# Performance work log

Hardware: AMD Instinct MI355X
Metric: run time of the kernel (lower is better)

Reference implementation:

```python
import jax, jax.numpy as jnp
import numpy as np

N_NODES = 100000
N_EDGES = 800000
F_IN = 128
HID = 128
HEADS = 4
HEAD_DIM = HID // HEADS
LAYERS = 3
N_CLASSES = 40
NEG_SLOPE = 0.2
BN_EPS = 1e-5


def setup_inputs() -> dict:
    key = jax.random.key(0)
    ks = jax.random.split(key, 10)
    feat = jax.random.normal(ks[0], (N_NODES, F_IN), dtype=jnp.float32)
    src = jax.random.randint(ks[1], (N_EDGES,), 0, N_NODES, dtype=jnp.int32)
    dst = jax.random.randint(ks[2], (N_EDGES,), 0, N_NODES, dtype=jnp.int32)
    W_enc = jax.random.normal(ks[3], (F_IN, HID), dtype=jnp.float32) / np.sqrt(F_IN)
    b_enc = jnp.zeros((HID,), dtype=jnp.float32)
    Ws = jax.random.normal(ks[4], (LAYERS, HID, HID), dtype=jnp.float32) / np.sqrt(HID)
    attn_ls = jax.random.normal(ks[5], (LAYERS, HEADS, HEAD_DIM), dtype=jnp.float32) / np.sqrt(HEAD_DIM)
    attn_rs = jax.random.normal(ks[6], (LAYERS, HEADS, HEAD_DIM), dtype=jnp.float32) / np.sqrt(HEAD_DIM)
    biases = jnp.zeros((LAYERS, HID), dtype=jnp.float32)
    gammas = jnp.ones((LAYERS, HID), dtype=jnp.float32)
    betas = jnp.zeros((LAYERS, HID), dtype=jnp.float32)
    W_pred = jax.random.normal(ks[7], (HID, N_CLASSES), dtype=jnp.float32) / np.sqrt(HID)
    b_pred = jnp.zeros((N_CLASSES,), dtype=jnp.float32)
    return {"feat": feat, "src": src, "dst": dst, "W_enc": W_enc, "b_enc": b_enc,
            "Ws": Ws, "attn_ls": attn_ls, "attn_rs": attn_rs, "biases": biases,
            "gammas": gammas, "betas": betas, "W_pred": W_pred, "b_pred": b_pred}


def _gat_layer(h, src, dst, W, a_l, a_r, bias, n_nodes):
    # h: [N, HID] -> projected per-head features [N, H, D]
    hf = (h @ W).reshape(n_nodes, HEADS, HEAD_DIM)
    el = jnp.sum(hf * a_l, axis=-1)  # [N, H]
    er = jnp.sum(hf * a_r, axis=-1)  # [N, H]
    e = jax.nn.leaky_relu(el[src] + er[dst], NEG_SLOPE)  # [E, H]
    # edge softmax over incoming edges of each destination node
    m = jax.ops.segment_max(e, dst, num_segments=n_nodes)  # [N, H]
    ex = jnp.exp(e - m[dst])
    s = jax.ops.segment_sum(ex, dst, num_segments=n_nodes)  # [N, H]
    alpha = ex / s[dst]  # [E, H]
    msg = hf[src] * alpha[:, :, None]  # [E, H, D]
    out = jax.ops.segment_sum(msg, dst, num_segments=n_nodes)  # [N, H, D]
    return out.reshape(n_nodes, HEADS * HEAD_DIM) + bias


def _batchnorm(x, gamma, beta):
    mean = jnp.mean(x, axis=0)
    var = jnp.var(x, axis=0)
    return gamma * (x - mean) * jax.lax.rsqrt(var + BN_EPS) + beta


def reference(feat, src, dst, W_enc, b_enc, Ws, attn_ls, attn_rs, biases, gammas, betas, W_pred, b_pred):
    n_nodes = feat.shape[0]
    h = jax.nn.relu(feat @ W_enc + b_enc)
    h_last = None
    for i in range(Ws.shape[0]):
        h = _gat_layer(h, src, dst, Ws[i], attn_ls[i], attn_rs[i], biases[i], n_nodes)
        if h_last is not None:
            h = h + h_last
        h_last = h
        h = _batchnorm(h, gammas[i], betas[i])
        h = jax.nn.relu(h)
    return h @ W_pred + b_pred
```

## Files before the change

### kernel.cpp

```cpp
#include <hip/hip_runtime.h>

typedef __attribute__((ext_vector_type(8))) short short8;
typedef __attribute__((ext_vector_type(4))) float f32x4;

#define N_NODES 100000
#define N_EDGES 800000
#define NEG 0.2f
#define BN_EPS 1e-5f
#define AGG_GRID 2048
#define MG_GRID 1024
#define MG_TILES 3125
#define SC_CHUNKS 256

__device__ __forceinline__ ushort bf16b(float f) {
  unsigned u = __float_as_uint(f);
  return (ushort)((u + 0x7FFFu + ((u >> 16) & 1u)) >> 16);
}
__device__ __forceinline__ float bflo(unsigned u) { return __uint_as_float(u << 16); }
__device__ __forceinline__ float bfhi(unsigned u) { return __uint_as_float(u & 0xFFFF0000u); }

__global__ void k_hist(const int* __restrict__ dst, int* __restrict__ cnt, int e) {
  int i = blockIdx.x * blockDim.x + threadIdx.x;
  if (i < e) atomicAdd(&cnt[dst[i]], 1);
}

__global__ void k_scan1(const int* __restrict__ cnt, int* __restrict__ rowptr,
                        int* __restrict__ bsums, int n) {
  __shared__ int sm[256];
  int i = blockIdx.x * 256 + threadIdx.x;
  int v = (i < n) ? cnt[i] : 0;
  sm[threadIdx.x] = v;
  __syncthreads();
  for (int off = 1; off < 256; off <<= 1) {
    int t = (threadIdx.x >= off) ? sm[threadIdx.x - off] : 0;
    __syncthreads();
    sm[threadIdx.x] += t;
    __syncthreads();
  }
  if (i < n) rowptr[i + 1] = sm[threadIdx.x];
  if (threadIdx.x == 255) bsums[blockIdx.x] = sm[255];
}

__global__ void k_scan2(int* __restrict__ bsums, int nb) {
  __shared__ int sm[512];
  int v = (threadIdx.x < nb) ? bsums[threadIdx.x] : 0;
  sm[threadIdx.x] = v;
  __syncthreads();
  for (int off = 1; off < 512; off <<= 1) {
    int t = (threadIdx.x >= off) ? sm[threadIdx.x - off] : 0;
    __syncthreads();
    sm[threadIdx.x] += t;
    __syncthreads();
  }
  if (threadIdx.x < nb) bsums[threadIdx.x] = sm[threadIdx.x] - v;
}

__global__ void k_scan3(int* __restrict__ rowptr, const int* __restrict__ bsums,
                        int* __restrict__ cursor, int n) {
  int i = blockIdx.x * 256 + threadIdx.x;
  if (i < n) {
    int val = rowptr[i + 1] + bsums[blockIdx.x];
    rowptr[i + 1] = val;
    if (i + 1 < n) cursor[i + 1] = val;
  }
  if (i == 0) { rowptr[0] = 0; cursor[0] = 0; }
}

__global__ __launch_bounds__(256) void k_scatter(
    const int* __restrict__ src, const int* __restrict__ dst,
    int* __restrict__ cursor, int2* __restrict__ esort, int e) {
  int xcd = blockIdx.x & 7;
  int chunk = blockIdx.x >> 3;
  int lo = xcd * (N_NODES / 8);
  int hi = lo + (N_NODES / 8);
  int per = (e + SC_CHUNKS - 1) / SC_CHUNKS;
  int beg = chunk * per;
  int end = min(e, beg + per);
  for (int i = beg + threadIdx.x; i < end; i += 256) {
    int d = dst[i];
    if (d >= lo && d < hi) {
      int pos = atomicAdd(&cursor[d], 1);
      esort[pos] = make_int2(src[i], d);
    }
  }
}

__global__ void k_packW(const float* __restrict__ W_enc, const float* __restrict__ Ws,
                        ushort* __restrict__ Wp) {
  int s = blockIdx.x * 256 + threadIdx.x;
  int wi = s >> 11, s2 = s & 2047;
  int kt = s2 >> 9, nb8 = (s2 >> 6) & 7, l = s2 & 63;
  const float* Wsrc = (wi == 0) ? W_enc : Ws + (size_t)(wi - 1) * 16384;
  int n = nb8 * 16 + (l & 15);
  int k0 = kt * 32 + (l >> 4) * 8;
  unsigned pk[4];
#pragma unroll
  for (int j = 0; j < 4; ++j) {
    ushort lo = bf16b(Wsrc[(size_t)(k0 + 2 * j) * 128 + n]);
    ushort hi = bf16b(Wsrc[(size_t)(k0 + 2 * j + 1) * 128 + n]);
    pk[j] = (unsigned)lo | ((unsigned)hi << 16);
  }
  *(uint4*)&Wp[(size_t)s * 8] = make_uint4(pk[0], pk[1], pk[2], pk[3]);
}

template <int MODE>
__global__ __launch_bounds__(256) void k_mgemm(
    const float* __restrict__ Af, const ushort* __restrict__ Ab,
    const ushort* __restrict__ Wp, const float* __restrict__ bias,
    const float* __restrict__ stats, const float* __restrict__ al,
    const float* __restrict__ ar, float* __restrict__ el, float* __restrict__ er,
    float4* __restrict__ blockmax, ushort* __restrict__ Cb) {
  __shared__ __align__(16) ushort Al[32 * 128];
  int tid = threadIdx.x;
  int lane = tid & 63, w = tid >> 6;
  int wr = w & 1, wc = w >> 1;
  int l15 = lane & 15, l4 = lane >> 4;

  const uint4* wp4 = (const uint4*)Wp;
  short8 bfr[4][4];
#pragma unroll
  for (int kt = 0; kt < 4; ++kt) {
#pragma unroll
    for (int nb = 0; nb < 4; ++nb) {
      uint4 t = wp4[(size_t)((kt * 8 + wc * 4 + nb) * 64 + lane)];
      bfr[kt][nb] = *(short8*)&t;
    }
  }

  float alv0 = 0, alv1 = 0, alv2 = 0, alv3 = 0;
  float arv0 = 0, arv1 = 0, arv2 = 0, arv3 = 0;
  float bv0 = 0, bv1 = 0, bv2 = 0, bv3 = 0;
  if (MODE != 0) {
    alv0 = al[64 * wc + l15];      arv0 = ar[64 * wc + l15];
    alv1 = al[64 * wc + 16 + l15]; arv1 = ar[64 * wc + 16 + l15];
    alv2 = al[64 * wc + 32 + l15]; arv2 = ar[64 * wc + 32 + l15];
    alv3 = al[64 * wc + 48 + l15]; arv3 = ar[64 * wc + 48 + l15];
  } else {
    bv0 = bias[64 * wc + l15];      bv1 = bias[64 * wc + 16 + l15];
    bv2 = bias[64 * wc + 32 + l15]; bv3 = bias[64 * wc + 48 + l15];
  }

  float gmx0 = -1e30f, gmx1 = -1e30f;

  int srow = tid >> 3;
  int c16 = (tid & 7) * 16;
  int kc0 = (tid & 7) * 2;
  int arow = 16 * wr + l15;
  const char* abase = (const char*)Al + arow * 256;
  int sw = arow & 7;

  for (int tile = blockIdx.x; tile < MG_TILES; tile += MG_GRID) {
    int rb = tile * 32;
    __syncthreads();
    {
      char* base = (char*)Al + srow * 256;
      if (MODE == 1) {
        const uint4* srcp = (const uint4*)(Ab + (size_t)(rb + srow) * 128 + c16);
        uint4 v0 = srcp[0], v1 = srcp[1];
        *(uint4*)(base + ((kc0 ^ (srow & 7)) << 4)) = v0;
        *(uint4*)(base + (((kc0 + 1) ^ (srow & 7)) << 4)) = v1;
      } else if (MODE == 2) {
        const uint4* srcp = (const uint4*)(Ab + (size_t)(rb + srow) * 128 + c16);
        uint4 v0 = srcp[0], v1 = srcp[1];
        unsigned pk[8];
#pragma unroll
        for (int j = 0; j < 4; ++j) {
          unsigned wv = ((const unsigned*)&v0)[j];
          float2 sc = *(const float2*)&stats[c16 + 2 * j];
          float2 sh = *(const float2*)&stats[128 + c16 + 2 * j];
          float x0 = fmaxf(bflo(wv) * sc.x + sh.x, 0.f);
          float x1 = fmaxf(bfhi(wv) * sc.y + sh.y, 0.f);
          pk[j] = (unsigned)bf16b(x0) | ((unsigned)bf16b(x1) << 16);
        }
#pragma unroll
        for (int j = 0; j < 4; ++j) {
          unsigned wv = ((const unsigned*)&v1)[j];
          float2 sc = *(const float2*)&stats[c16 + 8 + 2 * j];
          float2 sh = *(const float2*)&stats[128 + c16 + 8 + 2 * j];
          float x0 = fmaxf(bflo(wv) * sc.x + sh.x, 0.f);
          float x1 = fmaxf(bfhi(wv) * sc.y + sh.y, 0.f);
          pk[4 + j] = (unsigned)bf16b(x0) | ((unsigned)bf16b(x1) << 16);
        }
        *(uint4*)(base + ((kc0 ^ (srow & 7)) << 4)) = make_uint4(pk[0], pk[1], pk[2], pk[3]);
        *(uint4*)(base + (((kc0 + 1) ^ (srow & 7)) << 4)) = make_uint4(pk[4], pk[5], pk[6], pk[7]);
      } else {
        const float4* srcp = (const float4*)(Af + (size_t)(rb + srow) * 128 + c16);
        float4 f[4];
#pragma unroll
        for (int j = 0; j < 4; ++j) f[j] = srcp[j];
        unsigned pk[8];
#pragma unroll
        for (int j = 0; j < 4; ++j) {
          pk[2 * j] = (unsigned)bf16b(f[j].x) | ((unsigned)bf16b(f[j].y) << 16);
          pk[2 * j + 1] = (unsigned)bf16b(f[j].z) | ((unsigned)bf16b(f[j].w) << 16);
        }
        *(uint4*)(base + ((kc0 ^ (srow & 7)) << 4)) = make_uint4(pk[0], pk[1], pk[2], pk[3]);
        *(uint4*)(base + (((kc0 + 1) ^ (srow & 7)) << 4)) = make_uint4(pk[4], pk[5], pk[6], pk[7]);
      }
    }
    __syncthreads();

    f32x4 acc[4];
#pragma unroll
    for (int nb = 0; nb < 4; ++nb) acc[nb] = (f32x4){0.f, 0.f, 0.f, 0.f};
#pragma unroll
    for (int kt = 0; kt < 4; ++kt) {
      short8 af = *(const short8*)(abase + (((kt * 4 + l4) ^ sw) << 4));
      acc[0] = __builtin_amdgcn_mfma_f32_16x16x32_bf16(af, bfr[kt][0], acc[0], 0, 0, 0);
      acc[1] = __builtin_amdgcn_mfma_f32_16x16x32_bf16(af, bfr[kt][1], acc[1], 0, 0, 0);
      acc[2] = __builtin_amdgcn_mfma_f32_16x16x32_bf16(af, bfr[kt][2], acc[2], 0, 0, 0);
      acc[3] = __builtin_amdgcn_mfma_f32_16x16x32_bf16(af, bfr[kt][3], acc[3], 0, 0, 0);
    }

    int row0 = rb + 16 * wr + 4 * l4;
#pragma unroll
    for (int i = 0; i < 4; ++i) {
      int row = row0 + i;
      if (MODE != 0) {
        float pl0 = acc[0][i] * alv0 + acc[1][i] * alv1;
        float pr0 = acc[0][i] * arv0 + acc[1][i] * arv1;
        float pl1 = acc[2][i] * alv2 + acc[3][i] * alv3;
        float pr1 = acc[2][i] * arv2 + acc[3][i] * arv3;
#pragma unroll
        for (int o = 1; o < 16; o <<= 1) {
          pl0 += __shfl_xor(pl0, o); pr0 += __shfl_xor(pr0, o);
          pl1 += __shfl_xor(pl1, o); pr1 += __shfl_xor(pr1, o);
        }
        gmx0 = fmaxf(gmx0, pl0); gmx1 = fmaxf(gmx1, pl1);
        if (l15 == 0) {
          el[(size_t)row * 4 + 2 * wc] = pl0;     er[(size_t)row * 4 + 2 * wc] = pr0;
          el[(size_t)row * 4 + 2 * wc + 1] = pl1; er[(size_t)row * 4 + 2 * wc + 1] = pr1;
        }
      }
      float v0 = acc[0][i], v1 = acc[1][i], v2 = acc[2][i], v3 = acc[3][i];
      if (MODE == 0) {
        v0 = fmaxf(v0 + bv0, 0.f); v1 = fmaxf(v1 + bv1, 0.f);
        v2 = fmaxf(v2 + bv2, 0.f); v3 = fmaxf(v3 + bv3, 0.f);
      }
      size_t rbase = (size_t)row * 128 + 64 * wc + l15;
      Cb[rbase] = bf16b(v0);
      Cb[rbase + 16] = bf16b(v1);
      Cb[rbase + 32] = bf16b(v2);
      Cb[rbase + 48] = bf16b(v3);
    }
  }

  if (MODE != 0) {
    gmx0 = fmaxf(gmx0, __shfl_xor(gmx0, 16)); gmx0 = fmaxf(gmx0, __shfl_xor(gmx0, 32));
    gmx1 = fmaxf(gmx1, __shfl_xor(gmx1, 16)); gmx1 = fmaxf(gmx1, __shfl_xor(gmx1, 32));
    __shared__ float lm[4][2];
    if (lane == 0) { lm[w][0] = gmx0; lm[w][1] = gmx1; }
    __syncthreads();
    if (tid == 0) {
      float4 bm;
      bm.x = fmaxf(lm[0][0], lm[1][0]);
      bm.y = fmaxf(lm[0][1], lm[1][1]);
      bm.z = fmaxf(lm[2][0], lm[3][0]);
      bm.w = fmaxf(lm[2][1], lm[3][1]);
      blockmax[blockIdx.x] = bm;
    }
  }
}

__global__ __launch_bounds__(256) void k_elmax2(const float4* __restrict__ bm,
                                                float* __restrict__ elmax, int g) {
  float4 m = make_float4(-1e30f, -1e30f, -1e30f, -1e30f);
  for (int i = threadIdx.x; i < g; i += 256) {
    float4 v = bm[i];
    m.x = fmaxf(m.x, v.x); m.y = fmaxf(m.y, v.y);
    m.z = fmaxf(m.z, v.z); m.w = fmaxf(m.w, v.w);
  }
  __shared__ float4 sm[256];
  sm[threadIdx.x] = m;
  __syncthreads();
  for (int off = 128; off; off >>= 1) {
    if (threadIdx.x < off) {
      float4 o = sm[threadIdx.x + off];
      sm[threadIdx.x].x = fmaxf(sm[threadIdx.x].x, o.x);
      sm[threadIdx.x].y = fmaxf(sm[threadIdx.x].y, o.y);
      sm[threadIdx.x].z = fmaxf(sm[threadIdx.x].z, o.z);
      sm[threadIdx.x].w = fmaxf(sm[threadIdx.x].w, o.w);
    }
    __syncthreads();
  }
  if (threadIdx.x == 0) {
    elmax[0] = sm[0].x; elmax[1] = sm[0].y;
    elmax[2] = sm[0].z; elmax[3] = sm[0].w;
  }
}

__global__ __launch_bounds__(256) void k_edgew(
    const int2* __restrict__ esort, const float* __restrict__ el,
    const float* __restrict__ er, const float* __restrict__ elmax,
    float4* __restrict__ wgt, int e) {
  int j = blockIdx.x * 256 + threadIdx.x;
  if (j >= e) return;
  int2 sd = esort[j];
  float4 elv = *(const float4*)&el[(size_t)4 * sd.x];
  float4 erv = *(const float4*)&er[(size_t)4 * sd.y];
  float m0 = elmax[0] + erv.x;
  float m1 = elmax[1] + erv.y;
  float m2 = elmax[2] + erv.z;
  float m3 = elmax[3] + erv.w;
  m0 = fmaxf(m0, NEG * m0); m1 = fmaxf(m1, NEG * m1);
  m2 = fmaxf(m2, NEG * m2); m3 = fmaxf(m3, NEG * m3);
  float e0 = elv.x + erv.x; e0 = fmaxf(e0, NEG * e0);
  float e1 = elv.y + erv.y; e1 = fmaxf(e1, NEG * e1);
  float e2 = elv.z + erv.z; e2 = fmaxf(e2, NEG * e2);
  float e3 = elv.w + erv.w; e3 = fmaxf(e3, NEG * e3);
  float4 wv;
  wv.x = __expf(e0 - m0); wv.y = __expf(e1 - m1);
  wv.z = __expf(e2 - m2); wv.w = __expf(e3 - m3);
  wgt[j] = wv;
}

__global__ __launch_bounds__(256, 8) void k_aggregate(
    const ushort* __restrict__ hf, const float4* __restrict__ wgt,
    const int* __restrict__ rowptr, const int2* __restrict__ esort,
    const float* __restrict__ bias, ushort* __restrict__ hpre,
    float* __restrict__ part, int n, int addres) {
  int tid = threadIdx.x;
  int w = tid >> 6, lane = tid & 63;
  int h = lane >> 4;
  int c0 = 2 * lane;
  float2 bb = *(const float2*)&bias[c0];
  float sbn0 = 0.f, sbn1 = 0.f, qbn0 = 0.f, qbn1 = 0.f;
  for (int wid = blockIdx.x * 4 + w; wid < n; wid += AGG_GRID * 4) {
    int beg = rowptr[wid], end = rowptr[wid + 1];
    float s0 = 0.f, a00 = 0.f, a10 = 0.f;
    float s1 = 0.f, a01 = 0.f, a11 = 0.f;
    float s2 = 0.f, a02 = 0.f, a12 = 0.f;
    float s3 = 0.f, a03 = 0.f, a13 = 0.f;
    int j = beg;
    for (; j + 4 <= end; j += 4) {
      int sA = esort[j].x, sB = esort[j + 1].x, sC = esort[j + 2].x, sD = esort[j + 3].x;
      float wA = ((const float*)(wgt + j))[h];
      float wB = ((const float*)(wgt + j + 1))[h];
      float wC = ((const float*)(wgt + j + 2))[h];
      float wD = ((const float*)(wgt + j + 3))[h];
      unsigned hA = *(const unsigned*)(hf + (size_t)sA * 128 + c0);
      unsigned hB = *(const unsigned*)(hf + (size_t)sB * 128 + c0);
      unsigned hC = *(const unsigned*)(hf + (size_t)sC * 128 + c0);
      unsigned hD = *(const unsigned*)(hf + (size_t)sD * 128 + c0);
      s0 += wA; a00 += wA * bflo(hA); a10 += wA * bfhi(hA);
      s1 += wB; a01 += wB * bflo(hB); a11 += wB * bfhi(hB);
      s2 += wC; a02 += wC * bflo(hC); a12 += wC * bfhi(hC);
      s3 += wD; a03 += wD * bflo(hD); a13 += wD * bfhi(hD);
    }
    if (j < end) {
      int jB = (j + 1 < end) ? j + 1 : j;
      int jC = (j + 2 < end) ? j + 2 : j;
      int jD = (j + 3 < end) ? j + 3 : j;
      int sA = esort[j].x, sB = esort[jB].x, sC = esort[jC].x, sD = esort[jD].x;
      float wA = ((const float*)(wgt + j))[h];
      float wB = (j + 1 < end) ? ((const float*)(wgt + jB))[h] : 0.f;
      float wC = (j + 2 < end) ? ((const float*)(wgt + jC))[h] : 0.f;
      float wD = (j + 3 < end) ? ((const float*)(wgt + jD))[h] : 0.f;
      unsigned hA = *(const unsigned*)(hf + (size_t)sA * 128 + c0);
      unsigned hB = *(const unsigned*)(hf + (size_t)sB * 128 + c0);
      unsigned hC = *(const unsigned*)(hf + (size_t)sC * 128 + c0);
      unsigned hD = *(const unsigned*)(hf + (size_t)sD * 128 + c0);
      s0 += wA; a00 += wA * bflo(hA); a10 += wA * bfhi(hA);
      s1 += wB; a01 += wB * bflo(hB); a11 += wB * bfhi(hB);
      s2 += wC; a02 += wC * bflo(hC); a12 += wC * bfhi(hC);
      s3 += wD; a03 += wD * bflo(hD); a13 += wD * bfhi(hD);
    }
    float s = (s0 + s1) + (s2 + s3);
    float inv = (end > beg) ? 1.f / s : 0.f;
    float a0 = ((a00 + a01) + (a02 + a03)) * inv;
    float a1 = ((a10 + a11) + (a12 + a13)) * inv;
    float r0 = 0.f, r1 = 0.f;
    if (addres) {
      unsigned rr = *(const unsigned*)(hpre + (size_t)wid * 128 + c0);
      r0 = bflo(rr); r1 = bfhi(rr);
    }
    float o0 = a0 + bb.x + r0, o1 = a1 + bb.y + r1;
    *(unsigned*)(hpre + (size_t)wid * 128 + c0) =
        (unsigned)bf16b(o0) | ((unsigned)bf16b(o1) << 16);
    sbn0 += o0; qbn0 += o0 * o0;
    sbn1 += o1; qbn1 += o1 * o1;
  }
  __shared__ float red_s[4][128];
  __shared__ float red_q[4][128];
  red_s[w][c0] = sbn0; red_s[w][c0 + 1] = sbn1;
  red_q[w][c0] = qbn0; red_q[w][c0 + 1] = qbn1;
  __syncthreads();
  if (tid < 128)
    part[(size_t)blockIdx.x * 256 + tid] =
        (red_s[0][tid] + red_s[1][tid]) + (red_s[2][tid] + red_s[3][tid]);
  else if (tid < 256) {
    int c = tid - 128;
    part[(size_t)blockIdx.x * 256 + tid] =
        (red_q[0][c] + red_q[1][c]) + (red_q[2][c] + red_q[3][c]);
  }
}

__global__ __launch_bounds__(320) void k_pred(
    const ushort* __restrict__ A, const float* __restrict__ stats,
    const float* __restrict__ W, const float* __restrict__ bias,
    float* __restrict__ out, int n) {
  __shared__ float Wl[128 * 40];
  __shared__ float Xl[32 * 132];
  for (int i = threadIdx.x; i < 128 * 40; i += 320) Wl[i] = W[i];
  int cg = threadIdx.x % 10;
  int rg = threadIdx.x / 10;
  float4 bv = *(const float4*)&bias[4 * cg];
  for (int rb = blockIdx.x * 32; rb < n; rb += gridDim.x * 32) {
    __syncthreads();
    for (int idx = threadIdx.x; idx < 1024; idx += 320) {
      int r = idx >> 5, c = (idx & 31) * 4;
      uint2 v = *(const uint2*)(A + (size_t)(rb + r) * 128 + c);
      float4 sc = *(const float4*)&stats[c];
      float4 sh = *(const float4*)&stats[128 + c];
      float x0 = fmaxf(bflo(v.x) * sc.x + sh.x, 0.f);
      float x1 = fmaxf(bfhi(v.x) * sc.y + sh.y, 0.f);
      float x2 = fmaxf(bflo(v.y) * sc.z + sh.z, 0.f);
      float x3 = fmaxf(bfhi(v.y) * sc.w + sh.w, 0.f);
      *(float4*)&Xl[r * 132 + c] = make_float4(x0, x1, x2, x3);
    }
    __syncthreads();
    float a0 = 0.f, a1 = 0.f, a2 = 0.f, a3 = 0.f;
#pragma unroll 4
    for (int k = 0; k < 128; ++k) {
      float x = Xl[rg * 132 + k];
      float4 w = *(float4*)&Wl[k * 40 + 4 * cg];
      a0 += x * w.x; a1 += x * w.y; a2 += x * w.z; a3 += x * w.w;
    }
    float4 o = make_float4(a0 + bv.x, a1 + bv.y, a2 + bv.z, a3 + bv.w);
    *(float4*)&out[(size_t)(rb + rg) * 40 + 4 * cg] = o;
  }
}

__global__ __launch_bounds__(256) void k_bnred(
    const float* __restrict__ part, float* __restrict__ colsum,
    const float* __restrict__ gamma, const float* __restrict__ beta,
    float* __restrict__ stats, unsigned* __restrict__ ctr, int g, int n) {
  int v = blockIdx.x;
  float acc = 0.f;
  for (int b = threadIdx.x; b < g; b += 256) acc += part[(size_t)b * 256 + v];
  __shared__ float sm[256];
  sm[threadIdx.x] = acc;
  __syncthreads();
  for (int off = 128; off; off >>= 1) {
    if (threadIdx.x < off) sm[threadIdx.x] += sm[threadIdx.x + off];
    __syncthreads();
  }
  __shared__ int last;
  if (threadIdx.x == 0) {
    colsum[v] = sm[0];
    __threadfence();
    last = (atomicAdd(ctr, 1u) == (unsigned)(gridDim.x - 1));
  }
  __syncthreads();
  if (last) {
    __threadfence();
    if (threadIdx.x == 0) *ctr = 0;
    if (threadIdx.x < 128) {
      int c = threadIdx.x;
      float mean = colsum[c] / n;
      float var = colsum[128 + c] / n - mean * mean;
      float rstd = rsqrtf(var + BN_EPS);
      float scale = gamma[c] * rstd;
      stats[c] = scale;
      stats[128 + c] = beta[c] - mean * scale;
    }
  }
}

extern "C" void kernel_launch(void* const* d_in, const int* in_sizes, int n_in,
                              void* d_out, int out_size, void* d_ws, size_t ws_size,
                              hipStream_t stream) {
  const float* feat   = (const float*)d_in[0];
  const int*   src    = (const int*)d_in[1];
  const int*   dst    = (const int*)d_in[2];
  const float* W_enc  = (const float*)d_in[3];
  const float* b_enc  = (const float*)d_in[4];
  const float* Ws     = (const float*)d_in[5];
  const float* a_ls   = (const float*)d_in[6];
  const float* a_rs   = (const float*)d_in[7];
  const float* biases = (const float*)d_in[8];
  const float* gammas = (const float*)d_in[9];
  const float* betas  = (const float*)d_in[10];
  const float* W_pred = (const float*)d_in[11];
  const float* b_pred = (const float*)d_in[12];
  float* out = (float*)d_out;

  char* p = (char*)d_ws;
  auto alloc = [&](size_t bytes) {
    char* q = p;
    p += (bytes + 255) & ~(size_t)255;
    return q;
  };
  ushort* h_bf  = (ushort*)alloc((size_t)N_NODES * 128 * 2);
  ushort* hf_bf = (ushort*)alloc((size_t)N_NODES * 128 * 2);
  ushort* hpre  = (ushort*)alloc((size_t)N_NODES * 128 * 2);
  float* el     = (float*)alloc((size_t)N_NODES * 4 * 4);
  float* er     = (float*)alloc((size_t)N_NODES * 4 * 4);
  float* part   = (float*)alloc((size_t)AGG_GRID * 256 * 4);
  float* colsum = (float*)alloc(256 * 4);
  float* stats  = (float*)alloc(256 * 4);
  ushort* Wpack = (ushort*)alloc((size_t)4 * 2048 * 16);
  float4* bmax  = (float4*)alloc((size_t)MG_GRID * 16);
  float* elmax  = (float*)alloc(4 * 4);
  unsigned* ctr = (unsigned*)alloc(256);
  int* rowptr   = (int*)alloc((size_t)(N_NODES + 1) * 4);
  int* cursor   = (int*)alloc((size_t)N_NODES * 4);
  int* bsums    = (int*)alloc(512 * 4);
  int2* esort   = (int2*)alloc((size_t)N_EDGES * 8);
  float4* wgt   = (float4*)alloc((size_t)N_EDGES * 16);

  hipMemsetAsync(cursor, 0, (size_t)N_NODES * 4, stream);
  hipMemsetAsync(ctr, 0, 8, stream);
  k_hist<<<(N_EDGES + 255) / 256, 256, 0, stream>>>(dst, cursor, N_EDGES);
  int nb = (N_NODES + 255) / 256;
  k_scan1<<<nb, 256, 0, stream>>>(cursor, rowptr, bsums, N_NODES);
  k_scan2<<<1, 512, 0, stream>>>(bsums, nb);
  k_scan3<<<nb, 256, 0, stream>>>(rowptr, bsums, cursor, N_NODES);
  k_scatter<<<SC_CHUNKS * 8, 256, 0, stream>>>(src, dst, cursor, esort, N_EDGES);

  k_packW<<<32, 256, 0, stream>>>(W_enc, Ws, Wpack);

  k_mgemm<0><<<MG_GRID, 256, 0, stream>>>(feat, nullptr, Wpack, b_enc, nullptr, nullptr,
                                          nullptr, nullptr, nullptr, nullptr, h_bf);

  for (int L = 0; L < 3; ++L) {
    const float* al = a_ls + L * 128;
    const float* ar = a_rs + L * 128;
    const ushort* wp = Wpack + (size_t)(1 + L) * 16384;
    if (L == 0)
      k_mgemm<1><<<MG_GRID, 256, 0, stream>>>(nullptr, h_bf, wp, nullptr, nullptr, al,
                                              ar, el, er, bmax, hf_bf);
    else
      k_mgemm<2><<<MG_GRID, 256, 0, stream>>>(nullptr, hpre, wp, nullptr, stats, al,
                                              ar, el, er, bmax, hf_bf);
    k_elmax2<<<1, 256, 0, stream>>>(bmax, elmax, MG_GRID);
    k_edgew<<<(N_EDGES + 255) / 256, 256, 0, stream>>>(esort, el, er, elmax, wgt,
                                                       N_EDGES);
    k_aggregate<<<AGG_GRID, 256, 0, stream>>>(hf_bf, wgt, rowptr, esort,
                                              biases + L * 128, hpre, part, N_NODES,
                                              L > 0 ? 1 : 0);
    k_bnred<<<256, 256, 0, stream>>>(part, colsum, gammas + L * 128, betas + L * 128,
                                     stats, ctr, AGG_GRID, N_NODES);
  }
  k_pred<<<1563, 320, 0, stream>>>(hpre, stats, W_pred, b_pred, out, N_NODES);
}
```

Baseline: 407.6 us.

## Fuse encoder GEMM into first GAT projection and use MFMA for predictor

The encoder matmul and the layer-0 projection now run in one kernel. The ReLU'd encoder output stays in shared memory as bf16 instead of making a round trip through a global h buffer. The final predictor is rewritten as a bf16 MFMA GEMM with a packed, zero-padded W_pred, replacing the scalar FP32 LDS loop. The cost is more registers in the fused kernel, which holds two weight fragment sets, and bf16 rounding in the predictor.

```diff
diff --git a/kernel.cpp b/kernel.cpp
--- a/kernel.cpp
+++ b/kernel.cpp
@@ -103,6 +103,168 @@
   *(uint4*)&Wp[(size_t)s * 8] = make_uint4(pk[0], pk[1], pk[2], pk[3]);
 }
 
+__global__ void k_packP(const float* __restrict__ Wpred, ushort* __restrict__ Wp) {
+  int s = blockIdx.x * 256 + threadIdx.x;
+  if (s >= 1024) return;
+  int kt = s >> 8, nb = (s >> 6) & 3, l = s & 63;
+  int n = nb * 16 + (l & 15);
+  int k0 = kt * 32 + (l >> 4) * 8;
+  unsigned pk[4];
+#pragma unroll
+  for (int j = 0; j < 4; ++j) {
+    float lo = (n < 40) ? Wpred[(size_t)(k0 + 2 * j) * 40 + n] : 0.f;
+    float hi = (n < 40) ? Wpred[(size_t)(k0 + 2 * j + 1) * 40 + n] : 0.f;
+    pk[j] = (unsigned)bf16b(lo) | ((unsigned)bf16b(hi) << 16);
+  }
+  *(uint4*)&Wp[(size_t)s * 8] = make_uint4(pk[0], pk[1], pk[2], pk[3]);
+}
+
+__global__ __launch_bounds__(256) void k_fused(
+    const float* __restrict__ feat, const ushort* __restrict__ WpE,
+    const ushort* __restrict__ Wp0, const float* __restrict__ b_enc,
+    const float* __restrict__ al, const float* __restrict__ ar,
+    float* __restrict__ el, float* __restrict__ er,
+    float4* __restrict__ blockmax, ushort* __restrict__ Cb) {
+  __shared__ __align__(16) ushort Al[32 * 128];
+  __shared__ __align__(16) ushort A2[32 * 128];
+  int tid = threadIdx.x;
+  int lane = tid & 63, w = tid >> 6;
+  int wr = w & 1, wc = w >> 1;
+  int l15 = lane & 15, l4 = lane >> 4;
+
+  const uint4* wpE4 = (const uint4*)WpE;
+  const uint4* wp04 = (const uint4*)Wp0;
+  short8 bfrE[4][4], bfr0[4][4];
+#pragma unroll
+  for (int kt = 0; kt < 4; ++kt) {
+#pragma unroll
+    for (int nb = 0; nb < 4; ++nb) {
+      uint4 tE = wpE4[(size_t)((kt * 8 + wc * 4 + nb) * 64 + lane)];
+      bfrE[kt][nb] = *(short8*)&tE;
+      uint4 t0 = wp04[(size_t)((kt * 8 + wc * 4 + nb) * 64 + lane)];
+      bfr0[kt][nb] = *(short8*)&t0;
+    }
+  }
+
+  float bv0 = b_enc[64 * wc + l15],      bv1 = b_enc[64 * wc + 16 + l15];
+  float bv2 = b_enc[64 * wc + 32 + l15], bv3 = b_enc[64 * wc + 48 + l15];
+  float alv0 = al[64 * wc + l15],      arv0 = ar[64 * wc + l15];
+  float alv1 = al[64 * wc + 16 + l15], arv1 = ar[64 * wc + 16 + l15];
+  float alv2 = al[64 * wc + 32 + l15], arv2 = ar[64 * wc + 32 + l15];
+  float alv3 = al[64 * wc + 48 + l15], arv3 = ar[64 * wc + 48 + l15];
+
+  float gmx0 = -1e30f, gmx1 = -1e30f;
+  int srow = tid >> 3;
+  int c16 = (tid & 7) * 16;
+  int kc0 = (tid & 7) * 2;
+  int arow = 16 * wr + l15;
+  const char* abase = (const char*)Al + arow * 256;
+  const char* abase2 = (const char*)A2 + arow * 256;
+  int sw = arow & 7;
+
+  for (int tile = blockIdx.x; tile < MG_TILES; tile += MG_GRID) {
+    int rb = tile * 32;
+    __syncthreads();
+    {
+      char* base = (char*)Al + srow * 256;
+      const float4* srcp = (const float4*)(feat + (size_t)(rb + srow) * 128 + c16);
+      float4 f[4];
+#pragma unroll
+      for (int j = 0; j < 4; ++j) f[j] = srcp[j];
+      unsigned pk[8];
+#pragma unroll
+      for (int j = 0; j < 4; ++j) {
+        pk[2 * j] = (unsigned)bf16b(f[j].x) | ((unsigned)bf16b(f[j].y) << 16);
+        pk[2 * j + 1] = (unsigned)bf16b(f[j].z) | ((unsigned)bf16b(f[j].w) << 16);
+      }
+      *(uint4*)(base + ((kc0 ^ (srow & 7)) << 4)) = make_uint4(pk[0], pk[1], pk[2], pk[3]);
+      *(uint4*)(base + (((kc0 + 1) ^ (srow & 7)) << 4)) = make_uint4(pk[4], pk[5], pk[6], pk[7]);
+    }
+    __syncthreads();
+
+    f32x4 acc[4];
+#pragma unroll
+    for (int nb = 0; nb < 4; ++nb) acc[nb] = (f32x4){0.f, 0.f, 0.f, 0.f};
+#pragma unroll
+    for (int kt = 0; kt < 4; ++kt) {
+      short8 af = *(const short8*)(abase + (((kt * 4 + l4) ^ sw) << 4));
+      acc[0] = __builtin_amdgcn_mfma_f32_16x16x32_bf16(af, bfrE[kt][0], acc[0], 0, 0, 0);
+      acc[1] = __builtin_amdgcn_mfma_f32_16x16x32_bf16(af, bfrE[kt][1], acc[1], 0, 0, 0);
+      acc[2] = __builtin_amdgcn_mfma_f32_16x16x32_bf16(af, bfrE[kt][2], acc[2], 0, 0, 0);
+      acc[3] = __builtin_amdgcn_mfma_f32_16x16x32_bf16(af, bfrE[kt][3], acc[3], 0, 0, 0);
+    }
+    {
+      int rl0 = 16 * wr + 4 * l4;
+#pragma unroll
+      for (int i = 0; i < 4; ++i) {
+        int rl = rl0 + i;
+        int sw2 = rl & 7;
+        char* b2 = (char*)A2 + rl * 256;
+#pragma unroll
+        for (int nb = 0; nb < 4; ++nb) {
+          int col = 64 * wc + 16 * nb + l15;
+          float bv = (nb == 0) ? bv0 : (nb == 1) ? bv1 : (nb == 2) ? bv2 : bv3;
+          float v = fmaxf(acc[nb][i] + bv, 0.f);
+          int chunk = col >> 3;
+          *(ushort*)(b2 + (((chunk ^ sw2) << 4) | ((col & 7) * 2))) = bf16b(v);
+        }
+      }
+    }
+    __syncthreads();
+
+    f32x4 acc2[4];
+#pragma unroll
+    for (int nb = 0; nb < 4; ++nb) acc2[nb] = (f32x4){0.f, 0.f, 0.f, 0.f};
+#pragma unroll
+    for (int kt = 0; kt < 4; ++kt) {
+      short8 af = *(const short8*)(abase2 + (((kt * 4 + l4) ^ sw) << 4));
+      acc2[0] = __builtin_amdgcn_mfma_f32_16x16x32_bf16(af, bfr0[kt][0], acc2[0], 0, 0, 0);
+      acc2[1] = __builtin_amdgcn_mfma_f32_16x16x32_bf16(af, bfr0[kt][1], acc2[1], 0, 0, 0);
+      acc2[2] = __builtin_amdgcn_mfma_f32_16x16x32_bf16(af, bfr0[kt][2], acc2[2], 0, 0, 0);
+      acc2[3] = __builtin_amdgcn_mfma_f32_16x16x32_bf16(af, bfr0[kt][3], acc2[3], 0, 0, 0);
+    }
+
+    int row0 = rb + 16 * wr + 4 * l4;
+#pragma unroll
+    for (int i = 0; i < 4; ++i) {
+      int row = row0 + i;
+      float pl0 = acc2[0][i] * alv0 + acc2[1][i] * alv1;
+      float pr0 = acc2[0][i] * arv0 + acc2[1][i] * arv1;
+      float pl1 = acc2[2][i] * alv2 + acc2[3][i] * alv3;
+      float pr1 = acc2[2][i] * arv2 + acc2[3][i] * arv3;
+#pragma unroll
+      for (int o = 1; o < 16; o <<= 1) {
+        pl0 += __shfl_xor(pl0, o); pr0 += __shfl_xor(pr0, o);
+        pl1 += __shfl_xor(pl1, o); pr1 += __shfl_xor(pr1, o);
+      }
+      gmx0 = fmaxf(gmx0, pl0); gmx1 = fmaxf(gmx1, pl1);
+      if (l15 == 0) {
+        el[(size_t)row * 4 + 2 * wc] = pl0;     er[(size_t)row * 4 + 2 * wc] = pr0;
+        el[(size_t)row * 4 + 2 * wc + 1] = pl1; er[(size_t)row * 4 + 2 * wc + 1] = pr1;
+      }
+      size_t rbase = (size_t)row * 128 + 64 * wc + l15;
+      Cb[rbase] = bf16b(acc2[0][i]);
+      Cb[rbase + 16] = bf16b(acc2[1][i]);
+      Cb[rbase + 32] = bf16b(acc2[2][i]);
+      Cb[rbase + 48] = bf16b(acc2[3][i]);
+    }
+  }
+
+  gmx0 = fmaxf(gmx0, __shfl_xor(gmx0, 16)); gmx0 = fmaxf(gmx0, __shfl_xor(gmx0, 32));
+  gmx1 = fmaxf(gmx1, __shfl_xor(gmx1, 16)); gmx1 = fmaxf(gmx1, __shfl_xor(gmx1, 32));
+  __shared__ float lm[4][2];
+  if (lane == 0) { lm[w][0] = gmx0; lm[w][1] = gmx1; }
+  __syncthreads();
+  if (tid == 0) {
+    float4 bm;
+    bm.x = fmaxf(lm[0][0], lm[1][0]);
+    bm.y = fmaxf(lm[0][1], lm[1][1]);
+    bm.z = fmaxf(lm[2][0], lm[3][0]);
+    bm.w = fmaxf(lm[2][1], lm[3][1]);
+    blockmax[blockIdx.x] = bm;
+  }
+}
+
 template <int MODE>
 __global__ __launch_bounds__(256) void k_mgemm(
     const float* __restrict__ Af, const ushort* __restrict__ Ab,
@@ -127,21 +289,12 @@
     }
   }
 
-  float alv0 = 0, alv1 = 0, alv2 = 0, alv3 = 0;
-  float arv0 = 0, arv1 = 0, arv2 = 0, arv3 = 0;
-  float bv0 = 0, bv1 = 0, bv2 = 0, bv3 = 0;
-  if (MODE != 0) {
-    alv0 = al[64 * wc + l15];      arv0 = ar[64 * wc + l15];
-    alv1 = al[64 * wc + 16 + l15]; arv1 = ar[64 * wc + 16 + l15];
-    alv2 = al[64 * wc + 32 + l15]; arv2 = ar[64 * wc + 32 + l15];
-    alv3 = al[64 * wc + 48 + l15]; arv3 = ar[64 * wc + 48 + l15];
-  } else {
-    bv0 = bias[64 * wc + l15];      bv1 = bias[64 * wc + 16 + l15];
-    bv2 = bias[64 * wc + 32 + l15]; bv3 = bias[64 * wc + 48 + l15];
-  }
+  float alv0 = al[64 * wc + l15],      arv0 = ar[64 * wc + l15];
+  float alv1 = al[64 * wc + 16 + l15], arv1 = ar[64 * wc + 16 + l15];
+  float alv2 = al[64 * wc + 32 + l15], arv2 = ar[64 * wc + 32 + l15];
+  float alv3 = al[64 * wc + 48 + l15], arv3 = ar[64 * wc + 48 + l15];
 
   float gmx0 = -1e30f, gmx1 = -1e30f;
-
   int srow = tid >> 3;
   int c16 = (tid & 7) * 16;
   int kc0 = (tid & 7) * 2;
@@ -154,49 +307,29 @@
     __syncthreads();
     {
       char* base = (char*)Al + srow * 256;
-      if (MODE == 1) {
-        const uint4* srcp = (const uint4*)(Ab + (size_t)(rb + srow) * 128 + c16);
-        uint4 v0 = srcp[0], v1 = srcp[1];
-        *(uint4*)(base + ((kc0 ^ (srow & 7)) << 4)) = v0;
-        *(uint4*)(base + (((kc0 + 1) ^ (srow & 7)) << 4)) = v1;
-      } else if (MODE == 2) {
-        const uint4* srcp = (const uint4*)(Ab + (size_t)(rb + srow) * 128 + c16);
-        uint4 v0 = srcp[0], v1 = srcp[1];
-        unsigned pk[8];
-#pragma unroll
-        for (int j = 0; j < 4; ++j) {
-          unsigned wv = ((const unsigned*)&v0)[j];
-          float2 sc = *(const float2*)&stats[c16 + 2 * j];
-          float2 sh = *(const float2*)&stats[128 + c16 + 2 * j];
-          float x0 = fmaxf(bflo(wv) * sc.x + sh.x, 0.f);
-          float x1 = fmaxf(bfhi(wv) * sc.y + sh.y, 0.f);
-          pk[j] = (unsigned)bf16b(x0) | ((unsigned)bf16b(x1) << 16);
-        }
-#pragma unroll
-        for (int j = 0; j < 4; ++j) {
-          unsigned wv = ((const unsigned*)&v1)[j];
-          float2 sc = *(const float2*)&stats[c16 + 8 + 2 * j];
-          float2 sh = *(const float2*)&stats[128 + c16 + 8 + 2 * j];
-          float x0 = fmaxf(bflo(wv) * sc.x + sh.x, 0.f);
-          float x1 = fmaxf(bfhi(wv) * sc.y + sh.y, 0.f);
-          pk[4 + j] = (unsigned)bf16b(x0) | ((unsigned)bf16b(x1) << 16);
-        }
-        *(uint4*)(base + ((kc0 ^ (srow & 7)) << 4)) = make_uint4(pk[0], pk[1], pk[2], pk[3]);
-        *(uint4*)(base + (((kc0 + 1) ^ (srow & 7)) << 4)) = make_uint4(pk[4], pk[5], pk[6], pk[7]);
-      } else {
-        const float4* srcp = (const float4*)(Af + (size_t)(rb + srow) * 128 + c16);
-        float4 f[4];
-#pragma unroll
-        for (int j = 0; j < 4; ++j) f[j] = srcp[j];
-        unsigned pk[8];
-#pragma unroll
-        for (int j = 0; j < 4; ++j) {
-          pk[2 * j] = (unsigned)bf16b(f[j].x) | ((unsigned)bf16b(f[j].y) << 16);
-          pk[2 * j + 1] = (unsigned)bf16b(f[j].z) | ((unsigned)bf16b(f[j].w) << 16);
-        }
-        *(uint4*)(base + ((kc0 ^ (srow & 7)) << 4)) = make_uint4(pk[0], pk[1], pk[2], pk[3]);
-        *(uint4*)(base + (((kc0 + 1) ^ (srow & 7)) << 4)) = make_uint4(pk[4], pk[5], pk[6], pk[7]);
-      }
+      const uint4* srcp = (const uint4*)(Ab + (size_t)(rb + srow) * 128 + c16);
+      uint4 v0 = srcp[0], v1 = srcp[1];
+      unsigned pk[8];
+#pragma unroll
+      for (int j = 0; j < 4; ++j) {
+        unsigned wv = ((const unsigned*)&v0)[j];
+        float2 sc = *(const float2*)&stats[c16 + 2 * j];
+        float2 sh = *(const float2*)&stats[128 + c16 + 2 * j];
+        float x0 = fmaxf(bflo(wv) * sc.x + sh.x, 0.f);
+        float x1 = fmaxf(bfhi(wv) * sc.y + sh.y, 0.f);
+        pk[j] = (unsigned)bf16b(x0) | ((unsigned)bf16b(x1) << 16);
+      }
+#pragma unroll
+      for (int j = 0; j < 4; ++j) {
+        unsigned wv = ((const unsigned*)&v1)[j];
+        float2 sc = *(const float2*)&stats[c16 + 8 + 2 * j];
+        float2 sh = *(const float2*)&stats[128 + c16 + 8 + 2 * j];
+        float x0 = fmaxf(bflo(wv) * sc.x + sh.x, 0.f);
+        float x1 = fmaxf(bfhi(wv) * sc.y + sh.y, 0.f);
+        pk[4 + j] = (unsigned)bf16b(x0) | ((unsigned)bf16b(x1) << 16);
+      }
+      *(uint4*)(base + ((kc0 ^ (srow & 7)) << 4)) = make_uint4(pk[0], pk[1], pk[2], pk[3]);
+      *(uint4*)(base + (((kc0 + 1) ^ (srow & 7)) << 4)) = make_uint4(pk[4], pk[5], pk[6], pk[7]);
     }
     __syncthreads();
 
@@ -216,49 +349,40 @@
 #pragma unroll
     for (int i = 0; i < 4; ++i) {
       int row = row0 + i;
-      if (MODE != 0) {
-        float pl0 = acc[0][i] * alv0 + acc[1][i] * alv1;
-        float pr0 = acc[0][i] * arv0 + acc[1][i] * arv1;
-        float pl1 = acc[2][i] * alv2 + acc[3][i] * alv3;
-        float pr1 = acc[2][i] * arv2 + acc[3][i] * arv3;
-#pragma unroll
-        for (int o = 1; o < 16; o <<= 1) {
-          pl0 += __shfl_xor(pl0, o); pr0 += __shfl_xor(pr0, o);
-          pl1 += __shfl_xor(pl1, o); pr1 += __shfl_xor(pr1, o);
-        }
-        gmx0 = fmaxf(gmx0, pl0); gmx1 = fmaxf(gmx1, pl1);
-        if (l15 == 0) {
-          el[(size_t)row * 4 + 2 * wc] = pl0;     er[(size_t)row * 4 + 2 * wc] = pr0;
-          el[(size_t)row * 4 + 2 * wc + 1] = pl1; er[(size_t)row * 4 + 2 * wc + 1] = pr1;
-        }
-      }
-      float v0 = acc[0][i], v1 = acc[1][i], v2 = acc[2][i], v3 = acc[3][i];
-      if (MODE == 0) {
-        v0 = fmaxf(v0 + bv0, 0.f); v1 = fmaxf(v1 + bv1, 0.f);
-        v2 = fmaxf(v2 + bv2, 0.f); v3 = fmaxf(v3 + bv3, 0.f);
+      float pl0 = acc[0][i] * alv0 + acc[1][i] * alv1;
+      float pr0 = acc[0][i] * arv0 + acc[1][i] * arv1;
+      float pl1 = acc[2][i] * alv2 + acc[3][i] * alv3;
+      float pr1 = acc[2][i] * arv2 + acc[3][i] * arv3;
+#pragma unroll
+      for (int o = 1; o < 16; o <<= 1) {
+        pl0 += __shfl_xor(pl0, o); pr0 += __shfl_xor(pr0, o);
+        pl1 += __shfl_xor(pl1, o); pr1 += __shfl_xor(pr1, o);
+      }
+      gmx0 = fmaxf(gmx0, pl0); gmx1 = fmaxf(gmx1, pl1);
+      if (l15 == 0) {
+        el[(size_t)row * 4 + 2 * wc] = pl0;     er[(size_t)row * 4 + 2 * wc] = pr0;
+        el[(size_t)row * 4 + 2 * wc + 1] = pl1; er[(size_t)row * 4 + 2 * wc + 1] = pr1;
       }
       size_t rbase = (size_t)row * 128 + 64 * wc + l15;
-      Cb[rbase] = bf16b(v0);
-      Cb[rbase + 16] = bf16b(v1);
-      Cb[rbase + 32] = bf16b(v2);
-      Cb[rbase + 48] = bf16b(v3);
-    }
-  }
-
-  if (MODE != 0) {
-    gmx0 = fmaxf(gmx0, __shfl_xor(gmx0, 16)); gmx0 = fmaxf(gmx0, __shfl_xor(gmx0, 32));
-    gmx1 = fmaxf(gmx1, __shfl_xor(gmx1, 16)); gmx1 = fmaxf(gmx1, __shfl_xor(gmx1, 32));
-    __shared__ float lm[4][2];
-    if (lane == 0) { lm[w][0] = gmx0; lm[w][1] = gmx1; }
-    __syncthreads();
-    if (tid == 0) {
-      float4 bm;
-      bm.x = fmaxf(lm[0][0], lm[1][0]);
-      bm.y = fmaxf(lm[0][1], lm[1][1]);
-      bm.z = fmaxf(lm[2][0], lm[3][0]);
-      bm.w = fmaxf(lm[2][1], lm[3][1]);
-      blockmax[blockIdx.x] = bm;
-    }
+      Cb[rbase] = bf16b(acc[0][i]);
+      Cb[rbase + 16] = bf16b(acc[1][i]);
+      Cb[rbase + 32] = bf16b(acc[2][i]);
+      Cb[rbase + 48] = bf16b(acc[3][i]);
+    }
+  }
+
+  gmx0 = fmaxf(gmx0, __shfl_xor(gmx0, 16)); gmx0 = fmaxf(gmx0, __shfl_xor(gmx0, 32));
+  gmx1 = fmaxf(gmx1, __shfl_xor(gmx1, 16)); gmx1 = fmaxf(gmx1, __shfl_xor(gmx1, 32));
+  __shared__ float lm[4][2];
+  if (lane == 0) { lm[w][0] = gmx0; lm[w][1] = gmx1; }
+  __syncthreads();
+  if (tid == 0) {
+    float4 bm;
+    bm.x = fmaxf(lm[0][0], lm[1][0]);
+    bm.y = fmaxf(lm[0][1], lm[1][1]);
+    bm.z = fmaxf(lm[2][0], lm[3][0]);
+    bm.w = fmaxf(lm[2][1], lm[3][1]);
+    blockmax[blockIdx.x] = bm;
   }
 }
 
@@ -395,39 +519,84 @@
   }
 }
 
-__global__ __launch_bounds__(320) void k_pred(
+__global__ __launch_bounds__(256) void k_predm(
     const ushort* __restrict__ A, const float* __restrict__ stats,
-    const float* __restrict__ W, const float* __restrict__ bias,
-    float* __restrict__ out, int n) {
-  __shared__ float Wl[128 * 40];
-  __shared__ float Xl[32 * 132];
-  for (int i = threadIdx.x; i < 128 * 40; i += 320) Wl[i] = W[i];
-  int cg = threadIdx.x % 10;
-  int rg = threadIdx.x / 10;
-  float4 bv = *(const float4*)&bias[4 * cg];
-  for (int rb = blockIdx.x * 32; rb < n; rb += gridDim.x * 32) {
-    __syncthreads();
-    for (int idx = threadIdx.x; idx < 1024; idx += 320) {
-      int r = idx >> 5, c = (idx & 31) * 4;
-      uint2 v = *(const uint2*)(A + (size_t)(rb + r) * 128 + c);
-      float4 sc = *(const float4*)&stats[c];
-      float4 sh = *(const float4*)&stats[128 + c];
-      float x0 = fmaxf(bflo(v.x) * sc.x + sh.x, 0.f);
-      float x1 = fmaxf(bfhi(v.x) * sc.y + sh.y, 0.f);
-      float x2 = fmaxf(bflo(v.y) * sc.z + sh.z, 0.f);
-      float x3 = fmaxf(bfhi(v.y) * sc.w + sh.w, 0.f);
-      *(float4*)&Xl[r * 132 + c] = make_float4(x0, x1, x2, x3);
-    }
-    __syncthreads();
-    float a0 = 0.f, a1 = 0.f, a2 = 0.f, a3 = 0.f;
-#pragma unroll 4
-    for (int k = 0; k < 128; ++k) {
-      float x = Xl[rg * 132 + k];
-      float4 w = *(float4*)&Wl[k * 40 + 4 * cg];
-      a0 += x * w.x; a1 += x * w.y; a2 += x * w.z; a3 += x * w.w;
-    }
-    float4 o = make_float4(a0 + bv.x, a1 + bv.y, a2 + bv.z, a3 + bv.w);
-    *(float4*)&out[(size_t)(rb + rg) * 40 + 4 * cg] = o;
+    const ushort* __restrict__ Wp, const float* __restrict__ bias,
+    float* __restrict__ out) {
+  __shared__ __align__(16) ushort Al[32 * 128];
+  int tid = threadIdx.x;
+  int lane = tid & 63, w = tid >> 6;
+  int wr = w & 1, wc = w >> 1;
+  int l15 = lane & 15, l4 = lane >> 4;
+
+  const uint4* wp4 = (const uint4*)Wp;
+  short8 bfrP[4][2];
+#pragma unroll
+  for (int kt = 0; kt < 4; ++kt) {
+#pragma unroll
+    for (int n = 0; n < 2; ++n) {
+      uint4 t = wp4[(size_t)((kt * 4 + wc * 2 + n) * 64 + lane)];
+      bfrP[kt][n] = *(short8*)&t;
+    }
+  }
+  int col0 = 32 * wc + l15, col1 = 32 * wc + 16 + l15;
+  float bp0 = (col0 < 40) ? bias[col0] : 0.f;
+  float bp1 = (col1 < 40) ? bias[col1] : 0.f;
+
+  int srow = tid >> 3;
+  int c16 = (tid & 7) * 16;
+  int kc0 = (tid & 7) * 2;
+  int arow = 16 * wr + l15;
+  const char* abase = (const char*)Al + arow * 256;
+  int sw = arow & 7;
+
+  for (int tile = blockIdx.x; tile < MG_TILES; tile += MG_GRID) {
+    int rb = tile * 32;
+    __syncthreads();
+    {
+      char* base = (char*)Al + srow * 256;
+      const uint4* srcp = (const uint4*)(A + (size_t)(rb + srow) * 128 + c16);
+      uint4 v0 = srcp[0], v1 = srcp[1];
+      unsigned pk[8];
+#pragma unroll
+      for (int j = 0; j < 4; ++j) {
+        unsigned wv = ((const unsigned*)&v0)[j];
+        float2 sc = *(const float2*)&stats[c16 + 2 * j];
+        float2 sh = *(const float2*)&stats[128 + c16 + 2 * j];
+        float x0 = fmaxf(bflo(wv) * sc.x + sh.x, 0.f);
+        float x1 = fmaxf(bfhi(wv) * sc.y + sh.y, 0.f);
+        pk[j] = (unsigned)bf16b(x0) | ((unsigned)bf16b(x1) << 16);
+      }
+#pragma unroll
+      for (int j = 0; j < 4; ++j) {
+        unsigned wv = ((const unsigned*)&v1)[j];
+        float2 sc = *(const float2*)&stats[c16 + 8 + 2 * j];
+        float2 sh = *(const float2*)&stats[128 + c16 + 8 + 2 * j];
+        float x0 = fmaxf(bflo(wv) * sc.x + sh.x, 0.f);
+        float x1 = fmaxf(bfhi(wv) * sc.y + sh.y, 0.f);
+        pk[4 + j] = (unsigned)bf16b(x0) | ((unsigned)bf16b(x1) << 16);
+      }
+      *(uint4*)(base + ((kc0 ^ (srow & 7)) << 4)) = make_uint4(pk[0], pk[1], pk[2], pk[3]);
+      *(uint4*)(base + (((kc0 + 1) ^ (srow & 7)) << 4)) = make_uint4(pk[4], pk[5], pk[6], pk[7]);
+    }
+    __syncthreads();
+
+    f32x4 acc0 = (f32x4){0.f, 0.f, 0.f, 0.f};
+    f32x4 acc1 = (f32x4){0.f, 0.f, 0.f, 0.f};
+#pragma unroll
+    for (int kt = 0; kt < 4; ++kt) {
+      short8 af = *(const short8*)(abase + (((kt * 4 + l4) ^ sw) << 4));
+      acc0 = __builtin_amdgcn_mfma_f32_16x16x32_bf16(af, bfrP[kt][0], acc0, 0, 0, 0);
+      acc1 = __builtin_amdgcn_mfma_f32_16x16x32_bf16(af, bfrP[kt][1], acc1, 0, 0, 0);
+    }
+
+    int row0 = rb + 16 * wr + 4 * l4;
+#pragma unroll
+    for (int i = 0; i < 4; ++i) {
+      int row = row0 + i;
+      if (col0 < 40) out[(size_t)row * 40 + col0] = acc0[i] + bp0;
+      if (col1 < 40) out[(size_t)row * 40 + col1] = acc1[i] + bp1;
+    }
   }
 }
 
@@ -491,7 +660,6 @@
     p += (bytes + 255) & ~(size_t)255;
     return q;
   };
-  ushort* h_bf  = (ushort*)alloc((size_t)N_NODES * 128 * 2);
   ushort* hf_bf = (ushort*)alloc((size_t)N_NODES * 128 * 2);
   ushort* hpre  = (ushort*)alloc((size_t)N_NODES * 128 * 2);
   float* el     = (float*)alloc((size_t)N_NODES * 4 * 4);
@@ -500,6 +668,7 @@
   float* colsum = (float*)alloc(256 * 4);
   float* stats  = (float*)alloc(256 * 4);
   ushort* Wpack = (ushort*)alloc((size_t)4 * 2048 * 16);
+  ushort* Wppack= (ushort*)alloc((size_t)1024 * 16);
   float4* bmax  = (float4*)alloc((size_t)MG_GRID * 16);
   float* elmax  = (float*)alloc(4 * 4);
   unsigned* ctr = (unsigned*)alloc(256);
@@ -519,17 +688,15 @@
   k_scatter<<<SC_CHUNKS * 8, 256, 0, stream>>>(src, dst, cursor, esort, N_EDGES);
 
   k_packW<<<32, 256, 0, stream>>>(W_enc, Ws, Wpack);
-
-  k_mgemm<0><<<MG_GRID, 256, 0, stream>>>(feat, nullptr, Wpack, b_enc, nullptr, nullptr,
-                                          nullptr, nullptr, nullptr, nullptr, h_bf);
+  k_packP<<<4, 256, 0, stream>>>(W_pred, Wppack);
 
   for (int L = 0; L < 3; ++L) {
     const float* al = a_ls + L * 128;
     const float* ar = a_rs + L * 128;
     const ushort* wp = Wpack + (size_t)(1 + L) * 16384;
     if (L == 0)
-      k_mgemm<1><<<MG_GRID, 256, 0, stream>>>(nullptr, h_bf, wp, nullptr, nullptr, al,
-                                              ar, el, er, bmax, hf_bf);
+      k_fused<<<MG_GRID, 256, 0, stream>>>(feat, Wpack, wp, b_enc, al, ar, el, er,
+                                           bmax, hf_bf);
     else
       k_mgemm<2><<<MG_GRID, 256, 0, stream>>>(nullptr, hpre, wp, nullptr, stats, al,
                                               ar, el, er, bmax, hf_bf);
@@ -542,5 +709,5 @@
     k_bnred<<<256, 256, 0, stream>>>(part, colsum, gammas + L * 128, betas + L * 128,
                                      stats, ctr, AGG_GRID, N_NODES);
   }
-  k_pred<<<1563, 320, 0, stream>>>(hpre, stats, W_pred, b_pred, out, N_NODES);
-}
+  k_predm<<<MG_GRID, 256, 0, stream>>>(hpre, stats, Wppack, b_pred, out);
+}
```

Result: faster. 377.6 us (-7.4%).
